# Kernel optimization log

Measured on AMD Instinct MI355X. Metric: run time of the kernel, lower is better.

Reference implementation:

```python
import jax, jax.numpy as jnp
import numpy as np

EPS = 1e-5
COMMITMENT_WEIGHT = 1.0


def setup_inputs() -> dict:
    key = jax.random.key(0)
    k1, k2 = jax.random.split(key)
    x = jax.random.normal(k1, (4, 4096, 128), dtype=jnp.float32)
    codebook = jax.random.normal(k2, (8192, 128), dtype=jnp.float32)
    return {"x": x, "codebook": codebook}


def _layernorm(x):
    # LayerNorm over last dim, elementwise_affine=False, eps=1e-5
    mu = jnp.mean(x, axis=-1, keepdims=True)
    var = jnp.mean(jnp.square(x - mu), axis=-1, keepdims=True)
    return (x - mu) * jax.lax.rsqrt(var + EPS)


def reference(x, codebook):
    b, n, d = x.shape
    xn = _layernorm(x)                      # [b, n, d]
    flat = xn.reshape(b * n, d)             # [bn, d]
    x2 = jnp.sum(flat * flat, axis=-1, keepdims=True)          # [bn, 1]
    e2 = jnp.sum(codebook * codebook, axis=-1)                  # [K]
    dots = jnp.einsum('nd,kd->nk', flat, codebook)              # [bn, K]
    distances = x2 - 2.0 * dots + e2[None, :]                   # [bn, K]
    embed_ind = jnp.argmin(distances, axis=-1)                  # [bn]
    quantize = codebook[embed_ind].reshape(b, n, d)             # gather
    embed_ind = embed_ind.reshape(b, n)
    loss = jnp.mean(jnp.square(quantize - xn)) * COMMITMENT_WEIGHT
    # straight-through
    quantize_st = xn + jax.lax.stop_gradient(quantize - xn)
    return (quantize_st, embed_ind, loss)
```

## Files before the change

### kernel.cpp

```cpp
#include <hip/hip_runtime.h>
#include <hip/hip_fp16.h>
#include <math.h>

typedef _Float16 half8  __attribute__((ext_vector_type(8)));
typedef _Float16 half2v __attribute__((ext_vector_type(2)));
typedef float   floatx4 __attribute__((ext_vector_type(4)));

#define ROWS   16384
#define DIM    128
#define KCODES 8192
#define NSPLIT 16
#define MTILE  256
#define NT     32
#define NCHUNK ((KCODES / NSPLIT) / NT)
#define KSPLIT (KCODES / NSPLIT)
#define DELTA  0.5f

__device__ __forceinline__ void async_copy16(const void* src, void* dst_lds) {
  __builtin_amdgcn_global_load_lds((const __attribute__((address_space(1))) void*)src,
                                   (__attribute__((address_space(3))) void*)dst_lds,
                                   16, 0, 0);
}

__global__ __launch_bounds__(256) void prep_kernel(
    const float* __restrict__ cb, const float* __restrict__ x,
    _Float16* __restrict__ ehg, _Float16* __restrict__ elg,
    float* __restrict__ e2g, _Float16* __restrict__ xnh)
{
  int tid = threadIdx.x;
  int L = tid & 63;
  int bx = blockIdx.x;
  if (bx < KCODES / 4) {
    int row = bx * 4 + (tid >> 6);
    float2 v = ((const float2*)(cb + (size_t)row * DIM))[L];
    float s2 = v.x * v.x + v.y * v.y;
    #pragma unroll
    for (int m = 1; m < 64; m <<= 1) s2 += __shfl_xor(s2, m);
    if (L == 0) e2g[row] = -0.5f * s2;
    _Float16 h0 = (_Float16)v.x, h1 = (_Float16)v.y;
    half2v hi = {h0, h1};
    half2v lo = {(_Float16)(v.x - (float)h0), (_Float16)(v.y - (float)h1)};
    ((half2v*)(ehg + (size_t)row * DIM))[L] = hi;
    ((half2v*)(elg + (size_t)row * DIM))[L] = lo;
  } else {
    int row = (bx - KCODES / 4) * 4 + (tid >> 6);
    float2 xv = ((const float2*)(x + (size_t)row * DIM))[L];
    float s = xv.x + xv.y;
    #pragma unroll
    for (int m = 1; m < 64; m <<= 1) s += __shfl_xor(s, m);
    float mu = s * (1.0f / 128.0f);
    float dx = xv.x - mu, dy = xv.y - mu;
    float s2 = dx * dx + dy * dy;
    #pragma unroll
    for (int m = 1; m < 64; m <<= 1) s2 += __shfl_xor(s2, m);
    float rstd = 1.0f / sqrtf(s2 * (1.0f / 128.0f) + 1e-5f);
    half2v hv = {(_Float16)(dx * rstd), (_Float16)(dy * rstd)};
    ((half2v*)(xnh + (size_t)row * DIM))[L] = hv;
  }
}

__global__ __launch_bounds__(256, 2) void argmin_kernel(
    const _Float16* __restrict__ xnh, const _Float16* __restrict__ ehg,
    const _Float16* __restrict__ elg, const float* __restrict__ e2g,
    float* __restrict__ b1p, int* __restrict__ i1p,
    float* __restrict__ b2p, int* __restrict__ i2p)
{
  __shared__ _Float16 ebuf[3][2][NT][128];
  __shared__ float e2lds[KSPLIT];

  int tid = threadIdx.x;
  int w   = tid >> 6;
  int L   = tid & 63;
  int c   = L & 15;
  int q   = L >> 4;

  int bx = blockIdx.x;
  int mt = bx & (ROWS / MTILE - 1);
  int ns = bx >> 6;

  int rowbase = mt * MTILE + w * 64;
  int code0 = ns * KSPLIT;
  _Float16* lbase = &ebuf[0][0][0][0];

  auto stage = [&](int ch, int p) {
    int cbase = code0 + ch * NT;
    _Float16* lb = lbase + (size_t)p * 2 * NT * 128;
    #pragma unroll
    for (int it = 0; it < 4; ++it) {
      int cid = it * 256 + tid;
      int arr = cid >> 9;
      int lc  = cid & 511;
      int n   = lc >> 4;
      int kcs = lc & 15;
      int kc  = kcs ^ (n & 7);
      const _Float16* g = (arr ? elg : ehg) + (size_t)(cbase + n) * DIM + kc * 8;
      async_copy16(g, lb + (size_t)cid * 8);
    }
  };

  half8 ah[4][4];
  #pragma unroll
  for (int g = 0; g < 4; ++g) {
    const _Float16* xr = xnh + (size_t)(rowbase + g * 16 + c) * DIM;
    #pragma unroll
    for (int ks = 0; ks < 4; ++ks)
      ah[g][ks] = *(const half8*)(xr + ks * 32 + q * 8);
  }

  if (tid < KSPLIT / 4) async_copy16(e2g + code0 + tid * 4, e2lds + tid * 4);
  stage(0, 0);
  stage(1, 1);

  float b1[4][4], b2[4][4]; int i1[4][4], i2[4][4];
  #pragma unroll
  for (int g = 0; g < 4; ++g)
    #pragma unroll
    for (int r = 0; r < 4; ++r) {
      b1[g][r] = -3.4e38f; b2[g][r] = -3.4e38f;
      i1[g][r] = 0; i2[g][r] = 0;
    }

  int bc = 0;
  int bs = 2;
  for (int ch = 0; ch < NCHUNK; ++ch) {
    if (ch + 1 < NCHUNK) asm volatile("s_waitcnt vmcnt(4)" ::: "memory");
    else                 asm volatile("s_waitcnt vmcnt(0)" ::: "memory");
    __builtin_amdgcn_s_barrier();
    if (ch + 2 < NCHUNK) stage(ch + 2, bs);

    int cbase = code0 + ch * NT;
    float e2h[2];
    e2h[0] = e2lds[ch * NT + c];
    e2h[1] = e2lds[ch * NT + 16 + c];

    #pragma unroll
    for (int s = 0; s < 2; ++s) {
      int n = s * 16 + c;
      half8 bh[4], bl[4];
      #pragma unroll
      for (int ks = 0; ks < 4; ++ks) {
        int slot = ((ks * 4 + q) ^ (c & 7)) * 8;
        bh[ks] = *(const half8*)&ebuf[bc][0][n][slot];
        bl[ks] = *(const half8*)&ebuf[bc][1][n][slot];
      }
      int nn = cbase + n;
      #pragma unroll
      for (int g = 0; g < 4; ++g) {
        floatx4 acc = {e2h[s], e2h[s], e2h[s], e2h[s]};
        #pragma unroll
        for (int ks = 0; ks < 4; ++ks) {
          acc = __builtin_amdgcn_mfma_f32_16x16x32_f16(ah[g][ks], bh[ks], acc, 0, 0, 0);
          acc = __builtin_amdgcn_mfma_f32_16x16x32_f16(ah[g][ks], bl[ks], acc, 0, 0, 0);
        }
        #pragma unroll
        for (int r = 0; r < 4; ++r) {
          float t = acc[r];
          bool gt1 = t > b1[g][r];
          bool gt2 = t > b2[g][r];
          b2[g][r] = gt1 ? b1[g][r] : (gt2 ? t  : b2[g][r]);
          i2[g][r] = gt1 ? i1[g][r] : (gt2 ? nn : i2[g][r]);
          b1[g][r] = gt1 ? t  : b1[g][r];
          i1[g][r] = gt1 ? nn : i1[g][r];
        }
      }
    }
    bc = (bc == 2) ? 0 : bc + 1;
    bs = (bs == 2) ? 0 : bs + 1;
  }

  #pragma unroll
  for (int m = 1; m < 16; m <<= 1)
    #pragma unroll
    for (int g = 0; g < 4; ++g)
      #pragma unroll
      for (int r = 0; r < 4; ++r) {
        float ob1 = __shfl_xor(b1[g][r], m); int oi1 = __shfl_xor(i1[g][r], m);
        float ob2 = __shfl_xor(b2[g][r], m); int oi2 = __shfl_xor(i2[g][r], m);
        if (ob1 > b1[g][r]) {
          float nb2 = (b1[g][r] >= ob2) ? b1[g][r] : ob2;
          int   ni2 = (b1[g][r] >= ob2) ? i1[g][r] : oi2;
          b1[g][r] = ob1; i1[g][r] = oi1;
          b2[g][r] = nb2; i2[g][r] = ni2;
        } else {
          float nb2 = (ob1 >= b2[g][r]) ? ob1 : b2[g][r];
          int   ni2 = (ob1 >= b2[g][r]) ? oi1 : i2[g][r];
          b2[g][r] = nb2; i2[g][r] = ni2;
        }
      }
  if (c == 0) {
    #pragma unroll
    for (int g = 0; g < 4; ++g)
      #pragma unroll
      for (int r = 0; r < 4; ++r) {
        int row = rowbase + g * 16 + q * 4 + r;
        b1p[(size_t)row * NSPLIT + ns] = b1[g][r];
        i1p[(size_t)row * NSPLIT + ns] = i1[g][r];
        b2p[(size_t)row * NSPLIT + ns] = b2[g][r];
        i2p[(size_t)row * NSPLIT + ns] = i2[g][r];
      }
  }
}

__global__ __launch_bounds__(256) void gather_loss_kernel(
    const float* __restrict__ x, const float* __restrict__ cb,
    const float* __restrict__ e2g,
    const float* __restrict__ b1p, const int* __restrict__ i1p,
    const float* __restrict__ b2p, const int* __restrict__ i2p,
    float* __restrict__ out_q, float* __restrict__ out_ind,
    float* __restrict__ row_loss)
{
  int tid = threadIdx.x;
  int L = tid & 63;
  int row = blockIdx.x * 4 + (tid >> 6);

  int k  = L & 31;
  int qd = L >> 5;

  int ci = 0; float cv = -3.4e38f;
  if (L < 16)      { ci = i1p[(size_t)row * NSPLIT + L];        cv = b1p[(size_t)row * NSPLIT + L]; }
  else if (L < 32) { ci = i2p[(size_t)row * NSPLIT + (L - 16)]; cv = b2p[(size_t)row * NSPLIT + (L - 16)]; }
  int   idxk = __shfl(ci, k);
  float tvk  = __shfl(cv, k);

  float tmax = tvk;
  #pragma unroll
  for (int m = 1; m < 32; m <<= 1) tmax = fmaxf(tmax, __shfl_xor(tmax, m));
  bool keep = tvk >= tmax - DELTA;

  float2 xv = ((const float2*)(x + (size_t)row * DIM))[L];
  float s = xv.x + xv.y;
  #pragma unroll
  for (int m = 1; m < 64; m <<= 1) s += __shfl_xor(s, m);
  float mu = s * (1.0f / 128.0f);
  float dx = xv.x - mu, dy = xv.y - mu;
  float s2 = dx * dx + dy * dy;
  #pragma unroll
  for (int m = 1; m < 64; m <<= 1) s2 += __shfl_xor(s2, m);
  float rstd = 1.0f / sqrtf(s2 * (1.0f / 128.0f) + 1e-5f);

  float t = -3.4e38f;
  float p = 0.f;
  if (keep) {
    const float4* xr4 = (const float4*)(x  + (size_t)row  * DIM);
    const float4* er4 = (const float4*)(cb + (size_t)idxk * DIM);
    #pragma unroll
    for (int j = 0; j < 16; ++j) {
      float4 a = xr4[qd * 16 + j];
      float4 e = er4[qd * 16 + j];
      p += (a.x - mu) * e.x + (a.y - mu) * e.y + (a.z - mu) * e.z + (a.w - mu) * e.w;
    }
    p *= rstd;
  }
  p += __shfl_xor(p, 32);
  if (keep) t = p + e2g[idxk];

  int bi = idxk;
  #pragma unroll
  for (int m = 1; m < 32; m <<= 1) {
    float ot = __shfl_xor(t, m);
    int   oi = __shfl_xor(bi, m);
    if (ot > t || (ot == t && oi < bi)) { t = ot; bi = oi; }
  }

  float2 qv = ((const float2*)(cb + (size_t)bi * DIM))[L];
  ((float2*)out_q)[(size_t)row * 64 + L] = qv;
  float xn0 = dx * rstd, xn1 = dy * rstd;
  float e0 = qv.x - xn0, e1 = qv.y - xn1;
  float le = e0 * e0 + e1 * e1;
  #pragma unroll
  for (int m = 1; m < 64; m <<= 1) le += __shfl_xor(le, m);
  if (L == 0) {
    row_loss[row] = le;
    out_ind[row] = (float)bi;
  }
}

__global__ __launch_bounds__(1024) void loss_reduce_kernel(
    const float* __restrict__ row_loss, float* __restrict__ out_loss)
{
  __shared__ float sm[1024];
  int tid = threadIdx.x;
  float s = 0.f;
  for (int i = tid; i < ROWS; i += 1024) s += row_loss[i];
  sm[tid] = s; __syncthreads();
  for (int st = 512; st > 0; st >>= 1) {
    if (tid < st) sm[tid] += sm[tid + st];
    __syncthreads();
  }
  if (tid == 0) *out_loss = sm[0] * (1.0f / (float)(ROWS * DIM));
}

extern "C" void kernel_launch(void* const* d_in, const int* in_sizes, int n_in,
                              void* d_out, int out_size, void* d_ws, size_t ws_size,
                              hipStream_t stream)
{
  const float* x  = (const float*)d_in[0];
  const float* cb = (const float*)d_in[1];

  char* ws = (char*)d_ws;
  _Float16* ehg      = (_Float16*)(ws + 0);
  _Float16* elg      = (_Float16*)(ws + 2097152);
  float*    e2g      = (float*)   (ws + 4194304);
  int*      i1p      = (int*)     (ws + 4227072);
  int*      i2p      = (int*)     (ws + 5275648);
  float*    b1p      = (float*)   (ws + 6324224);
  float*    b2p      = (float*)   (ws + 7372800);
  float*    row_loss = (float*)   (ws + 8421376);

  float* out_q    = (float*)d_out;
  float* out_ind  = out_q + (size_t)ROWS * DIM;
  float* out_loss = out_ind + ROWS;

  _Float16* xnh = (_Float16*)out_q;

  prep_kernel<<<KCODES / 4 + ROWS / 4, 256, 0, stream>>>(cb, x, ehg, elg, e2g, xnh);
  argmin_kernel<<<(ROWS / MTILE) * NSPLIT, 256, 0, stream>>>(xnh, ehg, elg, e2g, b1p, i1p, b2p, i2p);
  gather_loss_kernel<<<ROWS / 4, 256, 0, stream>>>(x, cb, e2g, b1p, i1p, b2p, i2p, out_q, out_ind, row_loss);
  loss_reduce_kernel<<<1, 1024, 0, stream>>>(row_loss, out_loss);
}
```

Before: 179.1 us.

## Drop fp16 low-part split, pack group index into score bits, per-wave pipelines

Removes the hi/lo fp16 split of the codebook, so the screening GEMM runs half as many MFMAs and stages half the bytes. The top-2 tracking becomes unsigned max on float bits whose low 6 bits hold the group index; scores are offset by 256 to keep them positive. Each wave gets its own 3-deep LDS ring with no block barriers, and the codebook split drops from 16 to 8. The separate loss-reduce kernel is replaced by a per-block atomicAdd. The cost is lower screening precision (fp16-only codebook, truncated mantissa bits), which relies on the DELTA fp32 rescoring of top candidates to stay correct.

```diff
diff --git a/kernel.cpp b/kernel.cpp
--- a/kernel.cpp
+++ b/kernel.cpp
@@ -9,11 +9,10 @@
 #define ROWS   16384
 #define DIM    128
 #define KCODES 8192
-#define NSPLIT 16
+#define NSPLIT 8
+#define KSPLIT (KCODES / NSPLIT)
+#define NGROUP (KSPLIT / 16)
 #define MTILE  256
-#define NT     32
-#define NCHUNK ((KCODES / NSPLIT) / NT)
-#define KSPLIT (KCODES / NSPLIT)
 #define DELTA  0.5f
 
 __device__ __forceinline__ void async_copy16(const void* src, void* dst_lds) {
@@ -24,12 +23,13 @@
 
 __global__ __launch_bounds__(256) void prep_kernel(
     const float* __restrict__ cb, const float* __restrict__ x,
-    _Float16* __restrict__ ehg, _Float16* __restrict__ elg,
-    float* __restrict__ e2g, _Float16* __restrict__ xnh)
+    _Float16* __restrict__ ehg, float* __restrict__ e2g,
+    _Float16* __restrict__ xnh, float* __restrict__ out_loss)
 {
   int tid = threadIdx.x;
   int L = tid & 63;
   int bx = blockIdx.x;
+  if (bx == 0 && tid == 0) *out_loss = 0.f;
   if (bx < KCODES / 4) {
     int row = bx * 4 + (tid >> 6);
     float2 v = ((const float2*)(cb + (size_t)row * DIM))[L];
@@ -37,11 +37,8 @@
     #pragma unroll
     for (int m = 1; m < 64; m <<= 1) s2 += __shfl_xor(s2, m);
     if (L == 0) e2g[row] = -0.5f * s2;
-    _Float16 h0 = (_Float16)v.x, h1 = (_Float16)v.y;
-    half2v hi = {h0, h1};
-    half2v lo = {(_Float16)(v.x - (float)h0), (_Float16)(v.y - (float)h1)};
+    half2v hi = {(_Float16)v.x, (_Float16)v.y};
     ((half2v*)(ehg + (size_t)row * DIM))[L] = hi;
-    ((half2v*)(elg + (size_t)row * DIM))[L] = lo;
   } else {
     int row = (bx - KCODES / 4) * 4 + (tid >> 6);
     float2 xv = ((const float2*)(x + (size_t)row * DIM))[L];
@@ -61,42 +58,20 @@
 
 __global__ __launch_bounds__(256, 2) void argmin_kernel(
     const _Float16* __restrict__ xnh, const _Float16* __restrict__ ehg,
-    const _Float16* __restrict__ elg, const float* __restrict__ e2g,
+    const float* __restrict__ e2g,
     float* __restrict__ b1p, int* __restrict__ i1p,
     float* __restrict__ b2p, int* __restrict__ i2p)
 {
-  __shared__ _Float16 ebuf[3][2][NT][128];
-  __shared__ float e2lds[KSPLIT];
+  __shared__ _Float16 ebuf[4][3][16][128];
+  __shared__ float e2l[KSPLIT];
 
   int tid = threadIdx.x;
-  int w   = tid >> 6;
-  int L   = tid & 63;
-  int c   = L & 15;
-  int q   = L >> 4;
-
+  int w = tid >> 6, L = tid & 63, c = L & 15, q = L >> 4;
   int bx = blockIdx.x;
   int mt = bx & (ROWS / MTILE - 1);
   int ns = bx >> 6;
-
   int rowbase = mt * MTILE + w * 64;
   int code0 = ns * KSPLIT;
-  _Float16* lbase = &ebuf[0][0][0][0];
-
-  auto stage = [&](int ch, int p) {
-    int cbase = code0 + ch * NT;
-    _Float16* lb = lbase + (size_t)p * 2 * NT * 128;
-    #pragma unroll
-    for (int it = 0; it < 4; ++it) {
-      int cid = it * 256 + tid;
-      int arr = cid >> 9;
-      int lc  = cid & 511;
-      int n   = lc >> 4;
-      int kcs = lc & 15;
-      int kc  = kcs ^ (n & 7);
-      const _Float16* g = (arr ? elg : ehg) + (size_t)(cbase + n) * DIM + kc * 8;
-      async_copy16(g, lb + (size_t)cid * 8);
-    }
-  };
 
   half8 ah[4][4];
   #pragma unroll
@@ -107,98 +82,92 @@
       ah[g][ks] = *(const half8*)(xr + ks * 32 + q * 8);
   }
 
-  if (tid < KSPLIT / 4) async_copy16(e2g + code0 + tid * 4, e2lds + tid * 4);
-  stage(0, 0);
-  stage(1, 1);
-
-  float b1[4][4], b2[4][4]; int i1[4][4], i2[4][4];
+  {
+    float4 v = ((const float4*)(e2g + code0))[tid];
+    float4 o = {256.f + v.x, 256.f + v.y, 256.f + v.z, 256.f + v.w};
+    ((float4*)e2l)[tid] = o;
+  }
+  __syncthreads();
+
+  _Float16* wbase = &ebuf[w][0][0][0];
+  auto stage = [&](int g, int ring) {
+    int cbase = code0 + g * 16;
+    _Float16* lb = wbase + ring * (16 * 128);
+    #pragma unroll
+    for (int it = 0; it < 4; ++it) {
+      int cid = it * 64 + L;
+      int n   = cid >> 4;
+      int kcs = cid & 15;
+      int kc  = kcs ^ (n & 7);
+      async_copy16(ehg + (size_t)(cbase + n) * DIM + kc * 8, lb + cid * 8);
+    }
+  };
+  stage(0, 0); stage(1, 1); stage(2, 2);
+
+  unsigned k1[4][4], k2[4][4];
   #pragma unroll
   for (int g = 0; g < 4; ++g)
     #pragma unroll
+    for (int r = 0; r < 4; ++r) { k1[g][r] = 0u; k2[g][r] = 0u; }
+
+  for (int g = 0; g < NGROUP; ++g) {
+    if (g + 2 < NGROUP)      asm volatile("s_waitcnt vmcnt(8)" ::: "memory");
+    else if (g + 1 < NGROUP) asm volatile("s_waitcnt vmcnt(4)" ::: "memory");
+    else                     asm volatile("s_waitcnt vmcnt(0)" ::: "memory");
+
+    const _Float16* buf = wbase + (g % 3) * (16 * 128);
+    float e2v = e2l[(size_t)g * 16 + c];
+    half8 bh[4];
+    #pragma unroll
+    for (int ks = 0; ks < 4; ++ks)
+      bh[ks] = *(const half8*)(buf + (size_t)c * 128 + ((ks * 4 + q) ^ (c & 7)) * 8);
+
+    unsigned gp = (unsigned)g;
+    #pragma unroll
+    for (int gg = 0; gg < 4; ++gg) {
+      floatx4 acc = {e2v, e2v, e2v, e2v};
+      #pragma unroll
+      for (int ks = 0; ks < 4; ++ks)
+        acc = __builtin_amdgcn_mfma_f32_16x16x32_f16(ah[gg][ks], bh[ks], acc, 0, 0, 0);
+      #pragma unroll
+      for (int r = 0; r < 4; ++r) {
+        unsigned kk = (__float_as_uint(acc[r]) & 0xFFFFFFC0u) | gp;
+        unsigned tt = kk < k1[gg][r] ? kk : k1[gg][r];
+        k1[gg][r] = kk > k1[gg][r] ? kk : k1[gg][r];
+        k2[gg][r] = tt > k2[gg][r] ? tt : k2[gg][r];
+      }
+    }
+    asm volatile("s_waitcnt lgkmcnt(0)" ::: "memory");
+    if (g + 3 < NGROUP) stage(g + 3, g % 3);
+  }
+
+  #pragma unroll
+  for (int gg = 0; gg < 4; ++gg)
+    #pragma unroll
     for (int r = 0; r < 4; ++r) {
-      b1[g][r] = -3.4e38f; b2[g][r] = -3.4e38f;
-      i1[g][r] = 0; i2[g][r] = 0;
-    }
-
-  int bc = 0;
-  int bs = 2;
-  for (int ch = 0; ch < NCHUNK; ++ch) {
-    if (ch + 1 < NCHUNK) asm volatile("s_waitcnt vmcnt(4)" ::: "memory");
-    else                 asm volatile("s_waitcnt vmcnt(0)" ::: "memory");
-    __builtin_amdgcn_s_barrier();
-    if (ch + 2 < NCHUNK) stage(ch + 2, bs);
-
-    int cbase = code0 + ch * NT;
-    float e2h[2];
-    e2h[0] = e2lds[ch * NT + c];
-    e2h[1] = e2lds[ch * NT + 16 + c];
-
-    #pragma unroll
-    for (int s = 0; s < 2; ++s) {
-      int n = s * 16 + c;
-      half8 bh[4], bl[4];
+      float s1 = __uint_as_float(k1[gg][r] & 0xFFFFFFC0u) - 256.f;
+      float s2 = __uint_as_float(k2[gg][r] & 0xFFFFFFC0u) - 256.f;
+      int   j1 = code0 + (int)(k1[gg][r] & 63u) * 16 + c;
+      int   j2 = code0 + (int)(k2[gg][r] & 63u) * 16 + c;
       #pragma unroll
-      for (int ks = 0; ks < 4; ++ks) {
-        int slot = ((ks * 4 + q) ^ (c & 7)) * 8;
-        bh[ks] = *(const half8*)&ebuf[bc][0][n][slot];
-        bl[ks] = *(const half8*)&ebuf[bc][1][n][slot];
-      }
-      int nn = cbase + n;
-      #pragma unroll
-      for (int g = 0; g < 4; ++g) {
-        floatx4 acc = {e2h[s], e2h[s], e2h[s], e2h[s]};
-        #pragma unroll
-        for (int ks = 0; ks < 4; ++ks) {
-          acc = __builtin_amdgcn_mfma_f32_16x16x32_f16(ah[g][ks], bh[ks], acc, 0, 0, 0);
-          acc = __builtin_amdgcn_mfma_f32_16x16x32_f16(ah[g][ks], bl[ks], acc, 0, 0, 0);
-        }
-        #pragma unroll
-        for (int r = 0; r < 4; ++r) {
-          float t = acc[r];
-          bool gt1 = t > b1[g][r];
-          bool gt2 = t > b2[g][r];
-          b2[g][r] = gt1 ? b1[g][r] : (gt2 ? t  : b2[g][r]);
-          i2[g][r] = gt1 ? i1[g][r] : (gt2 ? nn : i2[g][r]);
-          b1[g][r] = gt1 ? t  : b1[g][r];
-          i1[g][r] = gt1 ? nn : i1[g][r];
+      for (int m = 1; m < 16; m <<= 1) {
+        float o1 = __shfl_xor(s1, m); int oj1 = __shfl_xor(j1, m);
+        float o2 = __shfl_xor(s2, m); int oj2 = __shfl_xor(j2, m);
+        if (o1 > s1) {
+          bool t = (s1 >= o2);
+          s2 = t ? s1 : o2;  j2 = t ? j1 : oj2;
+          s1 = o1; j1 = oj1;
+        } else {
+          bool t = (o1 >= s2);
+          s2 = t ? o1 : s2;  j2 = t ? oj1 : j2;
         }
       }
-    }
-    bc = (bc == 2) ? 0 : bc + 1;
-    bs = (bs == 2) ? 0 : bs + 1;
-  }
-
-  #pragma unroll
-  for (int m = 1; m < 16; m <<= 1)
-    #pragma unroll
-    for (int g = 0; g < 4; ++g)
-      #pragma unroll
-      for (int r = 0; r < 4; ++r) {
-        float ob1 = __shfl_xor(b1[g][r], m); int oi1 = __shfl_xor(i1[g][r], m);
-        float ob2 = __shfl_xor(b2[g][r], m); int oi2 = __shfl_xor(i2[g][r], m);
-        if (ob1 > b1[g][r]) {
-          float nb2 = (b1[g][r] >= ob2) ? b1[g][r] : ob2;
-          int   ni2 = (b1[g][r] >= ob2) ? i1[g][r] : oi2;
-          b1[g][r] = ob1; i1[g][r] = oi1;
-          b2[g][r] = nb2; i2[g][r] = ni2;
-        } else {
-          float nb2 = (ob1 >= b2[g][r]) ? ob1 : b2[g][r];
-          int   ni2 = (ob1 >= b2[g][r]) ? oi1 : i2[g][r];
-          b2[g][r] = nb2; i2[g][r] = ni2;
-        }
+      if (c == 0) {
+        int row = rowbase + gg * 16 + q * 4 + r;
+        b1p[(size_t)row * NSPLIT + ns] = s1; i1p[(size_t)row * NSPLIT + ns] = j1;
+        b2p[(size_t)row * NSPLIT + ns] = s2; i2p[(size_t)row * NSPLIT + ns] = j2;
       }
-  if (c == 0) {
-    #pragma unroll
-    for (int g = 0; g < 4; ++g)
-      #pragma unroll
-      for (int r = 0; r < 4; ++r) {
-        int row = rowbase + g * 16 + q * 4 + r;
-        b1p[(size_t)row * NSPLIT + ns] = b1[g][r];
-        i1p[(size_t)row * NSPLIT + ns] = i1[g][r];
-        b2p[(size_t)row * NSPLIT + ns] = b2[g][r];
-        i2p[(size_t)row * NSPLIT + ns] = i2[g][r];
-      }
-  }
+    }
 }
 
 __global__ __launch_bounds__(256) void gather_loss_kernel(
@@ -207,24 +176,26 @@
     const float* __restrict__ b1p, const int* __restrict__ i1p,
     const float* __restrict__ b2p, const int* __restrict__ i2p,
     float* __restrict__ out_q, float* __restrict__ out_ind,
-    float* __restrict__ row_loss)
-{
+    float* __restrict__ out_loss)
+{
+  __shared__ float lsum[4];
   int tid = threadIdx.x;
   int L = tid & 63;
-  int row = blockIdx.x * 4 + (tid >> 6);
-
-  int k  = L & 31;
-  int qd = L >> 5;
+  int w = tid >> 6;
+  int row = blockIdx.x * 4 + w;
+
+  int k  = L & 15;
+  int qd = L >> 4;
 
   int ci = 0; float cv = -3.4e38f;
-  if (L < 16)      { ci = i1p[(size_t)row * NSPLIT + L];        cv = b1p[(size_t)row * NSPLIT + L]; }
-  else if (L < 32) { ci = i2p[(size_t)row * NSPLIT + (L - 16)]; cv = b2p[(size_t)row * NSPLIT + (L - 16)]; }
+  if (L < 8)       { ci = i1p[(size_t)row * NSPLIT + L];       cv = b1p[(size_t)row * NSPLIT + L]; }
+  else if (L < 16) { ci = i2p[(size_t)row * NSPLIT + (L - 8)]; cv = b2p[(size_t)row * NSPLIT + (L - 8)]; }
   int   idxk = __shfl(ci, k);
   float tvk  = __shfl(cv, k);
 
   float tmax = tvk;
   #pragma unroll
-  for (int m = 1; m < 32; m <<= 1) tmax = fmaxf(tmax, __shfl_xor(tmax, m));
+  for (int m = 1; m < 16; m <<= 1) tmax = fmaxf(tmax, __shfl_xor(tmax, m));
   bool keep = tvk >= tmax - DELTA;
 
   float2 xv = ((const float2*)(x + (size_t)row * DIM))[L];
@@ -238,25 +209,25 @@
   for (int m = 1; m < 64; m <<= 1) s2 += __shfl_xor(s2, m);
   float rstd = 1.0f / sqrtf(s2 * (1.0f / 128.0f) + 1e-5f);
 
-  float t = -3.4e38f;
   float p = 0.f;
   if (keep) {
     const float4* xr4 = (const float4*)(x  + (size_t)row  * DIM);
     const float4* er4 = (const float4*)(cb + (size_t)idxk * DIM);
     #pragma unroll
-    for (int j = 0; j < 16; ++j) {
-      float4 a = xr4[qd * 16 + j];
-      float4 e = er4[qd * 16 + j];
+    for (int j = 0; j < 8; ++j) {
+      float4 a = xr4[qd * 8 + j];
+      float4 e = er4[qd * 8 + j];
       p += (a.x - mu) * e.x + (a.y - mu) * e.y + (a.z - mu) * e.z + (a.w - mu) * e.w;
     }
     p *= rstd;
   }
+  p += __shfl_xor(p, 16);
   p += __shfl_xor(p, 32);
-  if (keep) t = p + e2g[idxk];
+  float t = keep ? p + e2g[idxk] : -3.4e38f;
 
   int bi = idxk;
   #pragma unroll
-  for (int m = 1; m < 32; m <<= 1) {
+  for (int m = 1; m < 16; m <<= 1) {
     float ot = __shfl_xor(t, m);
     int   oi = __shfl_xor(bi, m);
     if (ot > t || (ot == t && oi < bi)) { t = ot; bi = oi; }
@@ -270,24 +241,12 @@
   #pragma unroll
   for (int m = 1; m < 64; m <<= 1) le += __shfl_xor(le, m);
   if (L == 0) {
-    row_loss[row] = le;
+    lsum[w] = le;
     out_ind[row] = (float)bi;
   }
-}
-
-__global__ __launch_bounds__(1024) void loss_reduce_kernel(
-    const float* __restrict__ row_loss, float* __restrict__ out_loss)
-{
-  __shared__ float sm[1024];
-  int tid = threadIdx.x;
-  float s = 0.f;
-  for (int i = tid; i < ROWS; i += 1024) s += row_loss[i];
-  sm[tid] = s; __syncthreads();
-  for (int st = 512; st > 0; st >>= 1) {
-    if (tid < st) sm[tid] += sm[tid + st];
-    __syncthreads();
-  }
-  if (tid == 0) *out_loss = sm[0] * (1.0f / (float)(ROWS * DIM));
+  __syncthreads();
+  if (tid == 0)
+    atomicAdd(out_loss, (lsum[0] + lsum[1] + lsum[2] + lsum[3]) * (1.0f / ((float)ROWS * DIM)));
 }
 
 extern "C" void kernel_launch(void* const* d_in, const int* in_sizes, int n_in,
@@ -298,14 +257,12 @@
   const float* cb = (const float*)d_in[1];
 
   char* ws = (char*)d_ws;
-  _Float16* ehg      = (_Float16*)(ws + 0);
-  _Float16* elg      = (_Float16*)(ws + 2097152);
-  float*    e2g      = (float*)   (ws + 4194304);
-  int*      i1p      = (int*)     (ws + 4227072);
-  int*      i2p      = (int*)     (ws + 5275648);
-  float*    b1p      = (float*)   (ws + 6324224);
-  float*    b2p      = (float*)   (ws + 7372800);
-  float*    row_loss = (float*)   (ws + 8421376);
+  _Float16* ehg = (_Float16*)(ws + 0);
+  float*    e2g = (float*)   (ws + 2097152);
+  float*    b1p = (float*)   (ws + 2129920);
+  int*      i1p = (int*)     (ws + 2654208);
+  float*    b2p = (float*)   (ws + 3178496);
+  int*      i2p = (int*)     (ws + 3702784);
 
   float* out_q    = (float*)d_out;
   float* out_ind  = out_q + (size_t)ROWS * DIM;
@@ -313,8 +270,7 @@
 
   _Float16* xnh = (_Float16*)out_q;
 
-  prep_kernel<<<KCODES / 4 + ROWS / 4, 256, 0, stream>>>(cb, x, ehg, elg, e2g, xnh);
-  argmin_kernel<<<(ROWS / MTILE) * NSPLIT, 256, 0, stream>>>(xnh, ehg, elg, e2g, b1p, i1p, b2p, i2p);
-  gather_loss_kernel<<<ROWS / 4, 256, 0, stream>>>(x, cb, e2g, b1p, i1p, b2p, i2p, out_q, out_ind, row_loss);
-  loss_reduce_kernel<<<1, 1024, 0, stream>>>(row_loss, out_loss);
-}
+  prep_kernel<<<KCODES / 4 + ROWS / 4, 256, 0, stream>>>(cb, x, ehg, e2g, xnh, out_loss);
+  argmin_kernel<<<(ROWS / MTILE) * NSPLIT, 256, 0, stream>>>(xnh, ehg, e2g, b1p, i1p, b2p, i2p);
+  gather_loss_kernel<<<ROWS / 4, 256, 0, stream>>>(x, cb, e2g, b1p, i1p, b2p, i2p, out_q, out_ind, out_loss);
+}
```

Measured after the change: 182.5 us. Within noise of the previous version (+1.9%).
